# Kernel optimization log

Measured on AMD Instinct MI355X. Metric: run time of the kernel, lower is better.

## Reference

```python
import jax, jax.numpy as jnp
import numpy as np

PATCH_PERCENTAGE = 0.5
THRESHOLD = 0.3
GAUSSIAN_STD = 0.25


def _center_of_gravity(line_drawing):
    # line_drawing: [B, 1, H, W]
    B, _, H, W = line_drawing.shape
    y = jnp.linspace(0.0, 1.0, H).reshape(1, 1, H, 1)
    x = jnp.linspace(0.0, 1.0, W).reshape(1, 1, 1, W)
    total = line_drawing.sum(axis=(2, 3)) + 1e-6          # [B, 1]
    cog_y = (line_drawing * y).sum(axis=(2, 3)) / total    # [B, 1]
    cog_x = (line_drawing * x).sum(axis=(2, 3)) / total    # [B, 1]
    return jnp.concatenate([cog_y, cog_x], axis=1)         # [B, 2] (y, x)


def _gaussian_weights(side, centers):
    # centers: [B, 2]; returns [B, side*side]
    lin = jnp.linspace(0.0, 1.0, side)
    gy, gx = jnp.meshgrid(lin, lin, indexing='ij')
    coords = jnp.stack([gy.ravel(), gx.ravel()], axis=1)   # [N, 2]
    d2 = ((coords[None, :, :] - centers[:, None, :]) ** 2).sum(-1)  # [B, N]
    return jnp.exp(-d2 / (2.0 * GAUSSIAN_STD ** 2))


def _selection_indices(scores, line_drawing, k):
    B, N = scores.shape
    side = int(np.sqrt(N))
    centers = _center_of_gravity(line_drawing)
    weights = _gaussian_weights(side, centers)
    weighted = scores * weights                            # [B, N]

    above = weighted > THRESHOLD                           # [B, N]
    count = above.sum(axis=1)                              # [B]
    idx = jnp.arange(N)

    # ascending above-threshold indices first (matches torch.where order)
    sort_key = jnp.where(above, idx[None, :], N + idx[None, :])
    above_sorted = jnp.argsort(sort_key, axis=1)[:, :k]    # [B, k]

    # top-k over below-threshold scores (above ones masked to -inf)
    masked = jnp.where(above, -jnp.inf, weighted)
    _, topk_masked = jax.lax.top_k(masked, k)              # [B, k]
    _, topk_all = jax.lax.top_k(weighted, k)               # [B, k]

    pos = jnp.arange(k)[None, :]                           # [1, k]
    shift = jnp.clip(pos - count[:, None], 0, k - 1)
    remaining = jnp.take_along_axis(topk_masked, shift, axis=1)
    combined = jnp.where(pos < count[:, None], above_sorted, remaining)

    use_topk = (count >= k) | (count == 0)                 # [B]
    return jnp.where(use_topk[:, None], topk_all, combined)


def setup_inputs() -> dict:
    key = jax.random.key(0)
    k1, k2, k3, k4 = jax.random.split(key, 4)
    B, N, D, HW = 64, 784, 768, 448
    return {
        'magno_patches': jax.random.normal(k1, (B, N, D), dtype=jnp.float32),
        'vit_positional_embedding': jax.random.normal(k2, (1, N + 1, D), dtype=jnp.float32),
        'scores': jax.random.uniform(k3, (B, N), dtype=jnp.float32),
        'line_drawing': jax.random.uniform(k4, (B, 1, HW, HW), dtype=jnp.float32),
    }


def reference(magno_patches, vit_positional_embedding, scores, line_drawing):
    B, N, D = magno_patches.shape
    k = int(N * PATCH_PERCENTAGE)
    sel = _selection_indices(scores, line_drawing, k)       # [B, k] int32

    sel_patches = jnp.take_along_axis(magno_patches, sel[:, :, None], axis=1)
    pos_embed = jnp.broadcast_to(vit_positional_embedding[:, 1:, :], (B, N, D))
    sel_pos = jnp.take_along_axis(pos_embed, sel[:, :, None], axis=1)
    return sel_patches + sel_pos
```

## Files before the change

kernel.cpp:

```cpp
#include <hip/hip_runtime.h>
#include <math.h>

#define BATCH 64
#define NPATCH 784
#define DIM 768
#define KSEL 392
#define SIDE 28
#define HWDIM 448
#define NPIX (HWDIM*HWDIM)
#define PARTS 49
#define PIX_PER_PART (NPIX/PARTS)
#define GSPLIT 4
#define IPB 196

typedef float f4v __attribute__((ext_vector_type(4)));
typedef unsigned long long u64;

__global__ __launch_bounds__(256) void cog_partial(const float* __restrict__ ld,
                                                   double* __restrict__ part) {
    const int blk = blockIdx.x;
    const int b = blk / PARTS;
    const int p = blk % PARTS;
    const int t = threadIdx.x;
    const int wid = t >> 6;
    const int lane = t & 63;

    __shared__ alignas(16) float lin[HWDIM];
    for (int e = t; e < HWDIM; e += 256) lin[e] = (float)((double)e / 447.0);
    __syncthreads();

    const float* base = ld + (size_t)b * NPIX + (size_t)p * PIX_PER_PART;
    double s = 0.0, sy = 0.0, sx = 0.0;

    #pragma unroll
    for (int r = 0; r < 4; ++r) {
        const int f4 = r * 256 + t;
        const int pix = p * PIX_PER_PART + f4 * 4;
        const f4v v = reinterpret_cast<const f4v*>(base)[f4];
        const int i = pix / HWDIM;
        const int j = pix - i * HWDIM;
        const float yf = lin[i];
        const f4v xq = *reinterpret_cast<const f4v*>(&lin[j]);
        s  += (double)v.x + (double)v.y + (double)v.z + (double)v.w;
        sy += (double)__fmul_rn(v.x, yf) + (double)__fmul_rn(v.y, yf)
            + (double)__fmul_rn(v.z, yf) + (double)__fmul_rn(v.w, yf);
        sx += (double)__fmul_rn(v.x, xq.x) + (double)__fmul_rn(v.y, xq.y)
            + (double)__fmul_rn(v.z, xq.z) + (double)__fmul_rn(v.w, xq.w);
    }

    #pragma unroll
    for (int off = 32; off > 0; off >>= 1) {
        s  += __shfl_down(s, off);
        sy += __shfl_down(sy, off);
        sx += __shfl_down(sx, off);
    }

    __shared__ double red[3][4];
    if (lane == 0) { red[0][wid] = s; red[1][wid] = sy; red[2][wid] = sx; }
    __syncthreads();
    if (t == 0) {
        double* dst = part + (size_t)(b * PARTS + p) * 3;
        dst[0] = (red[0][0] + red[0][1]) + (red[0][2] + red[0][3]);
        dst[1] = (red[1][0] + red[1][1]) + (red[1][2] + red[1][3]);
        dst[2] = (red[2][0] + red[2][1]) + (red[2][2] + red[2][3]);
    }
}

__global__ __launch_bounds__(256) void select_k(const float* __restrict__ scores,
                                                const double* __restrict__ part,
                                                int* __restrict__ sel) {
    const int blk = blockIdx.x;
    const int b = blk / GSPLIT;
    const int g = blk % GSPLIT;
    const int t = threadIdx.x;
    const int wid = t >> 6;
    const int lane = t & 63;

    __shared__ double sd[3][64];
    __shared__ float scog[2];
    __shared__ alignas(16) u64 skey[NPATCH];
    __shared__ u64 ajm[16];

    if (t < 64) {
        if (t < PARTS) {
            const double* src = part + (size_t)(b * PARTS + t) * 3;
            sd[0][t] = src[0]; sd[1][t] = src[1]; sd[2][t] = src[2];
        } else {
            sd[0][t] = 0.0; sd[1][t] = 0.0; sd[2][t] = 0.0;
        }
    }
    __syncthreads();
    for (int off = 32; off > 0; off >>= 1) {
        if (t < off) {
            sd[0][t] += sd[0][t + off];
            sd[1][t] += sd[1][t + off];
            sd[2][t] += sd[2][t + off];
        }
        __syncthreads();
    }
    if (t == 0) {
        const float total = __fadd_rn((float)sd[0][0], 1e-6f);
        scog[0] = __fdiv_rn((float)sd[1][0], total);
        scog[1] = __fdiv_rn((float)sd[2][0], total);
    }
    __syncthreads();
    const float cy = scog[0];
    const float cx = scog[1];

    #pragma unroll
    for (int pass = 0; pass < 4; ++pass) {
        const int n = pass * 256 + t;
        const bool valid = n < NPATCH;
        float wt = 0.0f;
        if (valid) {
            const int r = n / SIDE;
            const int c = n - r * SIDE;
            const float gy = (float)((double)r / 27.0);
            const float gx = (float)((double)c / 27.0);
            const float dy = gy - cy;
            const float dx = gx - cx;
            const float dy2 = __fmul_rn(dy, dy);
            const float dx2 = __fmul_rn(dx, dx);
            const float d2 = __fadd_rn(dy2, dx2);
            const float w = (float)exp((double)(-8.0f * d2));
            wt = __fmul_rn(scores[(size_t)b * NPATCH + n], w);
            skey[n] = ((u64)__float_as_uint(wt) << 10) | (u64)(1023 - n);
        }
        const u64 m = __ballot(valid && (wt > 0.3f));
        if (lane == 0) ajm[pass * 4 + wid] = m;
    }
    __syncthreads();

    const int i = g * IPB + t;
    if (t < IPB) {
        const u64 ki = skey[i];
        int r0 = 0, r1 = 0, r2 = 0, r3 = 0;
        #pragma unroll 4
        for (int j = 0; j < NPATCH; j += 4) {
            r0 += skey[j + 0] > ki;
            r1 += skey[j + 1] > ki;
            r2 += skey[j + 2] > ki;
            r3 += skey[j + 3] > ki;
        }
        const int r_all = (r0 + r1) + (r2 + r3);

        int count = 0;
        #pragma unroll
        for (int q = 0; q < 16; ++q) count += __popcll(ajm[q]);

        const int qi = i >> 6;
        const bool above_i = (ajm[qi] >> (u64)(i & 63)) & 1ull;
        int r_pre = 0;
        for (int q = 0; q < qi; ++q) r_pre += __popcll(ajm[q]);
        r_pre += __popcll(ajm[qi] & ((1ull << (u64)(i & 63)) - 1ull));

        const bool use_topk = (count == 0) || (count >= KSEL);
        const int dst = (!use_topk && above_i) ? r_pre : r_all;
        if (dst < KSEL) sel[(size_t)b * KSEL + dst] = i;
    }
}

__global__ __launch_bounds__(256) void gather_add(const float* __restrict__ magno,
                                                  const float* __restrict__ pos,
                                                  const int* __restrict__ sel,
                                                  float* __restrict__ out) {
    const int wid = threadIdx.x >> 6;
    const int lane = threadIdx.x & 63;
    const int w = blockIdx.x * 4 + wid;
    const int row0 = w * 2;
    const int row1 = row0 + 1;
    const int b0 = row0 / KSEL;
    const int b1 = row1 / KSEL;
    const int s0 = sel[row0];
    const int s1 = sel[row1];

    const f4v* src0 = reinterpret_cast<const f4v*>(magno + ((size_t)b0 * NPATCH + s0) * DIM);
    const f4v* src1 = reinterpret_cast<const f4v*>(magno + ((size_t)b1 * NPATCH + s1) * DIM);
    const f4v* pp0  = reinterpret_cast<const f4v*>(pos + (size_t)(s0 + 1) * DIM);
    const f4v* pp1  = reinterpret_cast<const f4v*>(pos + (size_t)(s1 + 1) * DIM);
    f4v* dst0 = reinterpret_cast<f4v*>(out + (size_t)row0 * DIM);
    f4v* dst1 = reinterpret_cast<f4v*>(out + (size_t)row1 * DIM);

    const f4v a0 = src0[lane], a1 = src0[64 + lane], a2 = src0[128 + lane];
    const f4v c0 = src1[lane], c1 = src1[64 + lane], c2 = src1[128 + lane];
    const f4v p0 = pp0[lane],  p1 = pp0[64 + lane],  p2 = pp0[128 + lane];
    const f4v q0 = pp1[lane],  q1 = pp1[64 + lane],  q2 = pp1[128 + lane];

    __builtin_nontemporal_store(a0 + p0, dst0 + lane);
    __builtin_nontemporal_store(a1 + p1, dst0 + 64 + lane);
    __builtin_nontemporal_store(a2 + p2, dst0 + 128 + lane);
    __builtin_nontemporal_store(c0 + q0, dst1 + lane);
    __builtin_nontemporal_store(c1 + q1, dst1 + 64 + lane);
    __builtin_nontemporal_store(c2 + q2, dst1 + 128 + lane);
}

extern "C" void kernel_launch(void* const* d_in, const int* in_sizes, int n_in,
                              void* d_out, int out_size, void* d_ws, size_t ws_size,
                              hipStream_t stream) {
    const float* magno  = (const float*)d_in[0];
    const float* vit    = (const float*)d_in[1];
    const float* scores = (const float*)d_in[2];
    const float* ld     = (const float*)d_in[3];
    float* out = (float*)d_out;

    double* partials = (double*)d_ws;
    int*    sel = (int*)((char*)d_ws + (size_t)BATCH * PARTS * 3 * sizeof(double));

    cog_partial<<<dim3(BATCH * PARTS), dim3(256), 0, stream>>>(ld, partials);
    select_k<<<dim3(BATCH * GSPLIT), dim3(256), 0, stream>>>(scores, partials, sel);
    gather_add<<<dim3(BATCH * KSEL / 8), dim3(256), 0, stream>>>(magno, vit, sel, out);
}
```

Before: 53.36 us.

## Fuse selection and gather into one kernel with split rank counting

Merges the select_k and gather_add kernels so each block computes ranks for its slice of patches and immediately copies the selected rows plus positional embeddings to their output slots. This removes one kernel launch and the round trip of the selection index array through global memory. The rank computation now splits each patch's comparison loop across 4 threads with a shared-memory reduction, and the grid grows to 16 blocks per batch. The cost is that every block redundantly recomputes the center of gravity, Gaussian weights and sort keys, with four times as many blocks doing that setup. Each block's gather is also limited to at most 49 rows handled by 4 wavefronts, so memory-level parallelism may be lower.

```diff
diff --git a/kernel.cpp b/kernel.cpp
--- a/kernel.cpp
+++ b/kernel.cpp
@@ -10,8 +10,8 @@
 #define NPIX (HWDIM*HWDIM)
 #define PARTS 49
 #define PIX_PER_PART (NPIX/PARTS)
-#define GSPLIT 4
-#define IPB 196
+#define GSPLIT 16
+#define IPB 49
 
 typedef float f4v __attribute__((ext_vector_type(4)));
 typedef unsigned long long u64;
@@ -66,9 +66,12 @@
     }
 }
 
-__global__ __launch_bounds__(256) void select_k(const float* __restrict__ scores,
-                                                const double* __restrict__ part,
-                                                int* __restrict__ sel) {
+__global__ __launch_bounds__(256) void select_gather(
+        const float* __restrict__ scores,
+        const double* __restrict__ part,
+        const float* __restrict__ magno,
+        const float* __restrict__ pos,
+        float* __restrict__ out) {
     const int blk = blockIdx.x;
     const int b = blk / GSPLIT;
     const int g = blk % GSPLIT;
@@ -80,6 +83,9 @@
     __shared__ float scog[2];
     __shared__ alignas(16) u64 skey[NPATCH];
     __shared__ u64 ajm[16];
+    __shared__ int sred[IPB * 4];
+    __shared__ unsigned spair[IPB];
+    __shared__ int snsel;
 
     if (t < 64) {
         if (t < PARTS) {
@@ -131,67 +137,69 @@
     }
     __syncthreads();
 
-    const int i = g * IPB + t;
-    if (t < IPB) {
-        const u64 ki = skey[i];
+    if (t < IPB * 4) {
+        const int e = t >> 2;
+        const int q = t & 3;
+        const u64 ki = skey[g * IPB + e];
+        const int j0 = q * 196;
         int r0 = 0, r1 = 0, r2 = 0, r3 = 0;
         #pragma unroll 4
-        for (int j = 0; j < NPATCH; j += 4) {
+        for (int j = j0; j < j0 + 196; j += 4) {
             r0 += skey[j + 0] > ki;
             r1 += skey[j + 1] > ki;
             r2 += skey[j + 2] > ki;
             r3 += skey[j + 3] > ki;
         }
-        const int r_all = (r0 + r1) + (r2 + r3);
-
-        int count = 0;
-        #pragma unroll
-        for (int q = 0; q < 16; ++q) count += __popcll(ajm[q]);
-
-        const int qi = i >> 6;
-        const bool above_i = (ajm[qi] >> (u64)(i & 63)) & 1ull;
-        int r_pre = 0;
-        for (int q = 0; q < qi; ++q) r_pre += __popcll(ajm[q]);
-        r_pre += __popcll(ajm[qi] & ((1ull << (u64)(i & 63)) - 1ull));
-
-        const bool use_topk = (count == 0) || (count >= KSEL);
-        const int dst = (!use_topk && above_i) ? r_pre : r_all;
-        if (dst < KSEL) sel[(size_t)b * KSEL + dst] = i;
-    }
-}
-
-__global__ __launch_bounds__(256) void gather_add(const float* __restrict__ magno,
-                                                  const float* __restrict__ pos,
-                                                  const int* __restrict__ sel,
-                                                  float* __restrict__ out) {
-    const int wid = threadIdx.x >> 6;
-    const int lane = threadIdx.x & 63;
-    const int w = blockIdx.x * 4 + wid;
-    const int row0 = w * 2;
-    const int row1 = row0 + 1;
-    const int b0 = row0 / KSEL;
-    const int b1 = row1 / KSEL;
-    const int s0 = sel[row0];
-    const int s1 = sel[row1];
-
-    const f4v* src0 = reinterpret_cast<const f4v*>(magno + ((size_t)b0 * NPATCH + s0) * DIM);
-    const f4v* src1 = reinterpret_cast<const f4v*>(magno + ((size_t)b1 * NPATCH + s1) * DIM);
-    const f4v* pp0  = reinterpret_cast<const f4v*>(pos + (size_t)(s0 + 1) * DIM);
-    const f4v* pp1  = reinterpret_cast<const f4v*>(pos + (size_t)(s1 + 1) * DIM);
-    f4v* dst0 = reinterpret_cast<f4v*>(out + (size_t)row0 * DIM);
-    f4v* dst1 = reinterpret_cast<f4v*>(out + (size_t)row1 * DIM);
-
-    const f4v a0 = src0[lane], a1 = src0[64 + lane], a2 = src0[128 + lane];
-    const f4v c0 = src1[lane], c1 = src1[64 + lane], c2 = src1[128 + lane];
-    const f4v p0 = pp0[lane],  p1 = pp0[64 + lane],  p2 = pp0[128 + lane];
-    const f4v q0 = pp1[lane],  q1 = pp1[64 + lane],  q2 = pp1[128 + lane];
-
-    __builtin_nontemporal_store(a0 + p0, dst0 + lane);
-    __builtin_nontemporal_store(a1 + p1, dst0 + 64 + lane);
-    __builtin_nontemporal_store(a2 + p2, dst0 + 128 + lane);
-    __builtin_nontemporal_store(c0 + q0, dst1 + lane);
-    __builtin_nontemporal_store(c1 + q1, dst1 + 64 + lane);
-    __builtin_nontemporal_store(c2 + q2, dst1 + 128 + lane);
+        sred[t] = (r0 + r1) + (r2 + r3);
+    }
+    __syncthreads();
+
+    if (t < 64) {
+        int mydst = KSEL;
+        int mysrc = 0;
+        if (t < IPB) {
+            const int i = g * IPB + t;
+            const int r_all = (sred[t * 4] + sred[t * 4 + 1])
+                            + (sred[t * 4 + 2] + sred[t * 4 + 3]);
+
+            int count = 0;
+            #pragma unroll
+            for (int q = 0; q < 16; ++q) count += __popcll(ajm[q]);
+
+            const int qi = i >> 6;
+            const bool above_i = (ajm[qi] >> (u64)(i & 63)) & 1ull;
+            int r_pre = 0;
+            for (int q = 0; q < qi; ++q) r_pre += __popcll(ajm[q]);
+            r_pre += __popcll(ajm[qi] & ((1ull << (u64)(i & 63)) - 1ull));
+
+            const bool use_topk = (count == 0) || (count >= KSEL);
+            mydst = (!use_topk && above_i) ? r_pre : r_all;
+            mysrc = i;
+        }
+        const bool selme = mydst < KSEL;
+        const u64 mask = __ballot(selme);
+        if (selme) {
+            const int posi = __popcll(mask & ((1ull << (u64)t) - 1ull));
+            spair[posi] = ((unsigned)mysrc << 16) | (unsigned)mydst;
+        }
+        if (t == 0) snsel = (int)__popcll(mask);
+    }
+    __syncthreads();
+
+    const int nsel = snsel;
+    for (int e = wid; e < nsel; e += 4) {
+        const unsigned pr = spair[e];
+        const int srcn = (int)(pr >> 16);
+        const int dslot = (int)(pr & 0xffffu);
+        const f4v* src = reinterpret_cast<const f4v*>(magno + ((size_t)b * NPATCH + srcn) * DIM);
+        const f4v* pp  = reinterpret_cast<const f4v*>(pos + (size_t)(srcn + 1) * DIM);
+        f4v* dq = reinterpret_cast<f4v*>(out + ((size_t)b * KSEL + dslot) * DIM);
+        const f4v a0 = src[lane], a1 = src[64 + lane], a2 = src[128 + lane];
+        const f4v p0 = pp[lane],  p1 = pp[64 + lane],  p2 = pp[128 + lane];
+        __builtin_nontemporal_store(a0 + p0, dq + lane);
+        __builtin_nontemporal_store(a1 + p1, dq + 64 + lane);
+        __builtin_nontemporal_store(a2 + p2, dq + 128 + lane);
+    }
 }
 
 extern "C" void kernel_launch(void* const* d_in, const int* in_sizes, int n_in,
@@ -204,9 +212,8 @@
     float* out = (float*)d_out;
 
     double* partials = (double*)d_ws;
-    int*    sel = (int*)((char*)d_ws + (size_t)BATCH * PARTS * 3 * sizeof(double));
 
     cog_partial<<<dim3(BATCH * PARTS), dim3(256), 0, stream>>>(ld, partials);
-    select_k<<<dim3(BATCH * GSPLIT), dim3(256), 0, stream>>>(scores, partials, sel);
-    gather_add<<<dim3(BATCH * KSEL / 8), dim3(256), 0, stream>>>(magno, vit, sel, out);
+    select_gather<<<dim3(BATCH * GSPLIT), dim3(256), 0, stream>>>(scores, partials,
+                                                                  magno, vit, out);
 }
```

Result: faster. 47.41 us, median of 2 (-11.2%).
